# Kernel tuning notes

Measured on AMD Instinct MI355X. Metric: run time of the kernel, lower is better.

## Reference

```python
import jax, jax.numpy as jnp
import numpy as np

K = 8              # kernel_size
C_IN = 3           # input_channels
HID = 256          # hidden_state_size
MID = 256          # mid_layer_size
N_MAIN = 4         # num_main_layers
N_CLS = 1000       # num_classes
N_PIX = K * K      # num_pixel_values
IN_VEC = 2 + 1 + N_PIX * C_IN + HID   # 451
OUT_VEC = 2 + 1 + HID                 # 259
B, H, W = 128, 256, 256


def _lin_init(k, fan_in, fan_out):
    kw, kb = jax.random.split(k)
    bound = 1.0 / np.sqrt(fan_in)
    w = jax.random.uniform(kw, (fan_in, fan_out), jnp.float32, -bound, bound)
    b = jax.random.uniform(kb, (fan_out,), jnp.float32, -bound, bound)
    return w, b


def setup_inputs() -> dict:
    key = jax.random.key(0)
    ks = jax.random.split(key, 16)
    image = jax.random.normal(ks[0], (B, C_IN, H, W), jnp.float32)
    locations = jax.random.uniform(ks[1], (B, 2), jnp.float32)
    scales = jax.random.uniform(ks[2], (B, 1), jnp.float32)
    hidden_state = jax.random.normal(ks[3], (B, HID), jnp.float32)
    w0, b0 = _lin_init(ks[4], IN_VEC, MID)
    rws, rbs = [], []
    for i in range(N_MAIN):
        w, b = _lin_init(jax.random.fold_in(ks[5], i), MID, MID)
        rws.append(w); rbs.append(b)
    rw = jnp.stack(rws); rb = jnp.stack(rbs)          # [4,MID,MID], [4,MID]
    wf, bf = _lin_init(ks[6], MID, OUT_VEC)
    cw0, cb0 = _lin_init(ks[7], HID, MID)
    crw, crb = _lin_init(ks[8], MID, MID)
    cw1, cb1 = _lin_init(ks[9], MID, N_CLS)
    return {"image": image, "locations": locations, "scales": scales,
            "hidden_state": hidden_state, "w0": w0, "b0": b0, "rw": rw,
            "rb": rb, "wf": wf, "bf": bf, "cw0": cw0, "cb0": cb0,
            "crw": crw, "crb": crb, "cw1": cw1, "cb1": cb1}


def fourier_interp_2d(image, sample_points):
    """Band-limited (NUDFT) interpolation of image at continuous points.
    image: [B,C,H,W]; sample_points: [B,N,2] in normalized [0,1) (ij order).
    Returns [B,N,C]."""
    Bsz, C, Hh, Ww = image.shape
    F = jnp.fft.fft2(image)                       # [B,C,H,W] complex
    fy = jnp.fft.fftfreq(Hh) * Hh                 # integer freqs [H]
    fx = jnp.fft.fftfreq(Ww) * Ww                 # integer freqs [W]
    y = sample_points[..., 0]                     # [B,N]
    x = sample_points[..., 1]
    two_pi_i = 2j * jnp.pi
    Ey = jnp.exp(two_pi_i * y[..., None] * fy)    # [B,N,H]
    Ex = jnp.exp(two_pi_i * x[..., None] * fx)    # [B,N,W]
    tmp = jnp.einsum('bchw,bnh->bcnw', F, Ey)     # dominant compute
    vals = jnp.einsum('bcnw,bnw->bcn', tmp, Ex).real / (Hh * Ww)
    return jnp.transpose(vals, (0, 2, 1))         # [B,N,C]


def reference(image, locations, scales, hidden_state,
              w0, b0, rw, rb, wf, bf, cw0, cb0, crw, crb, cw1, cb1):
    Bsz = image.shape[0]
    # base meshgrid: [K,K,2], ij indexing, values arange(K)/K
    g = jnp.arange(K, dtype=image.dtype) / K
    mesh = jnp.stack(jnp.meshgrid(g, g, indexing='ij'), axis=-1)  # [K,K,2]
    coords = mesh[None] - locations[:, None, None, :]             # [B,K,K,2]
    coords = coords * scales[:, None, None, :]
    coords = coords.reshape(Bsz, N_PIX, 2)
    pix = fourier_interp_2d(image, coords)                        # [B,N,C]
    pix = pix.reshape(Bsz, N_PIX * C_IN)
    inp = jnp.concatenate([locations, scales, pix, hidden_state], axis=-1)
    h = inp @ w0 + b0
    for i in range(N_MAIN):
        h = jax.nn.relu(h @ rw[i] + rb[i] + h)
    out = jnp.tanh(h @ wf + bf)                                   # [B,OUT_VEC]
    new_loc = locations + out[:, :2]
    new_scale = scales + out[:, 2:3]
    new_hidden = hidden_state + out[:, 3:]
    c = jax.nn.relu(new_hidden @ cw0 + cb0)
    c = jax.nn.relu(c @ crw + crb + c)
    preds = jax.nn.softmax(c @ cw1 + cb1, axis=-1)
    # concat all outputs: [B, 2+1+HID+N_CLS]
    return jnp.concatenate([new_loc, new_scale, new_hidden, preds], axis=-1)
```

## Files before the change

### kernel.cpp

```cpp
#include <hip/hip_runtime.h>
#include <math.h>

#define BB 128
#define OUTROW 1259

typedef float vf4 __attribute__((ext_vector_type(4)));

__device__ __forceinline__ ushort f2b(float x) {
    unsigned u = __float_as_uint(x);
    unsigned r = (u + 0x7FFFu + ((u >> 16) & 1u)) >> 16;
    return (ushort)r;
}
__device__ __forceinline__ float b2f(ushort b) {
    return __uint_as_float(((unsigned)b) << 16);
}
__device__ __forceinline__ float4 bf4tof(ushort4 u) {
    float4 f;
    f.x = __uint_as_float((unsigned)u.x << 16);
    f.y = __uint_as_float((unsigned)u.y << 16);
    f.z = __uint_as_float((unsigned)u.z << 16);
    f.w = __uint_as_float((unsigned)u.w << 16);
    return f;
}

#define OFF_W0   0u
#define OFF_RW   115456u
#define OFF_CW0  377600u
#define OFF_CRW  443136u
#define OFF_CW1  508672u
#define OFF_WF   764672u
#define N_CONV   831232u

__device__ __forceinline__ void dirichlet_ab(float t, float& A, float& Bv) {
    float r = t - rintf(t);
    float s256 = sinpif(256.0f * r);
    Bv = s256 * (1.0f / 256.0f);
    if (fabsf(r) < 1e-6f) {
        A = 1.0f;
    } else {
        float sp = sinpif(r), cp = cospif(r);
        A = Bv * cp / sp;
    }
}

__global__ __launch_bounds__(256) void interp_convert_kernel(
    const float* __restrict__ image, const float* __restrict__ loc,
    const float* __restrict__ scl, float* __restrict__ pix,
    const float* __restrict__ w0, const float* __restrict__ rw,
    const float* __restrict__ wf, const float* __restrict__ cw0,
    const float* __restrict__ crw, const float* __restrict__ cw1,
    ushort* __restrict__ bfa)
{
    __shared__ float U[256 * 16];
    __shared__ float V[16 * 260];
    __shared__ float T[16 * 260];

    int bid = blockIdx.x;
    int tid = threadIdx.x;

    if (bid >= 384) {
        unsigned g = (unsigned)(bid - 384) * 256u + (unsigned)tid;
        for (unsigned i = g; i < N_CONV; i += 2048u * 256u) {
            unsigned j = i; float v;
            if (j < 115456u) { v = w0[j]; bfa[OFF_W0 + j] = f2b(v); continue; }
            j -= 115456u;
            if (j < 262144u) { v = rw[j]; bfa[OFF_RW + j] = f2b(v); continue; }
            j -= 262144u;
            if (j < 65536u) { v = cw0[j]; bfa[OFF_CW0 + j] = f2b(v); continue; }
            j -= 65536u;
            if (j < 65536u) { v = crw[j]; bfa[OFF_CRW + j] = f2b(v); continue; }
            j -= 65536u;
            if (j < 256000u) { v = cw1[j]; bfa[OFF_CW1 + j] = f2b(v); continue; }
            j -= 256000u;
            {
                unsigned k = j / 260u, c = j - k * 260u;
                bfa[OFF_WF + j] = (c < 259u) ? f2b(wf[k * 259u + c]) : (ushort)0;
            }
        }
        return;
    }

    int b = bid / 3, c = bid % 3;
    float l0 = loc[2 * b], l1 = loc[2 * b + 1], sc = scl[b];

    {
        int p = tid;
        float tp = (float)p * (1.0f / 256.0f);
        #pragma unroll
        for (int iy = 0; iy < 8; ++iy) {
            float A, Bv;
            float y = ((float)iy * 0.125f - l0) * sc;
            dirichlet_ab(y - tp, A, Bv);
            int w = iy >> 1, o = iy & 1;
            U[p * 16 + w * 4 + o] = A;
            U[p * 16 + w * 4 + 2 + o] = Bv;
            float x = ((float)iy * 0.125f - l1) * sc;
            dirichlet_ab(x - tp, A, Bv);
            V[iy * 260 + p] = A;
            V[(8 + iy) * 260 + p] = Bv;
        }
    }
    __syncthreads();

    int wave = tid >> 6, lane = tid & 63;
    const float* img = image + (size_t)(b * 3 + c) * 65536 + lane * 4;

    float aA0[4] = {0, 0, 0, 0}, aA1[4] = {0, 0, 0, 0};
    float aB0[4] = {0, 0, 0, 0}, aB1[4] = {0, 0, 0, 0};
    #pragma unroll 4
    for (int p = 0; p < 256; ++p) {
        vf4 v = __builtin_nontemporal_load((const vf4*)(img + p * 256));
        const float4 u = *(const float4*)(&U[p * 16 + wave * 4]);
        aA0[0] += u.x * v[0]; aA0[1] += u.x * v[1]; aA0[2] += u.x * v[2]; aA0[3] += u.x * v[3];
        aA1[0] += u.y * v[0]; aA1[1] += u.y * v[1]; aA1[2] += u.y * v[2]; aA1[3] += u.y * v[3];
        aB0[0] += u.z * v[0]; aB0[1] += u.z * v[1]; aB0[2] += u.z * v[2]; aB0[3] += u.z * v[3];
        aB1[0] += u.w * v[0]; aB1[1] += u.w * v[1]; aB1[2] += u.w * v[2]; aB1[3] += u.w * v[3];
    }
    int iy0 = wave * 2;
    int q0 = lane * 4;
    #pragma unroll
    for (int j = 0; j < 4; ++j) {
        T[iy0 * 260 + q0 + j]       = aA0[j];
        T[(iy0 + 1) * 260 + q0 + j] = aA1[j];
        T[(8 + iy0) * 260 + q0 + j]     = aB0[j];
        T[(8 + iy0 + 1) * 260 + q0 + j] = aB1[j];
    }
    __syncthreads();

    int n = tid >> 2, sub = tid & 3;
    int iy = n >> 3, ix = n & 7;
    float s = 0.f;
    #pragma unroll 8
    for (int i = 0; i < 64; ++i) {
        int q = sub + 4 * i;
        s += T[iy * 260 + q] * V[ix * 260 + q] - T[(8 + iy) * 260 + q] * V[(8 + ix) * 260 + q];
    }
    s += __shfl_xor(s, 1);
    s += __shfl_xor(s, 2);
    if (sub == 0) pix[(b * 64 + n) * 3 + c] = s;
}

__device__ __forceinline__ void gemv256b(const ushort* __restrict__ W,
                                         const float* __restrict__ s_src,
                                         float* __restrict__ s_part,
                                         int sub, int j4)
{
    ushort4 wv[16];
    float hv[16];
    #pragma unroll
    for (int t = 0; t < 16; ++t)
        wv[t] = *(const ushort4*)(W + (size_t)(sub + 16 * t) * 256 + j4);
    #pragma unroll
    for (int t = 0; t < 16; ++t)
        hv[t] = s_src[sub + 16 * t];
    float4 a = {0.f, 0.f, 0.f, 0.f};
    #pragma unroll
    for (int t = 0; t < 16; ++t) {
        float4 w = bf4tof(wv[t]);
        a.x += hv[t] * w.x; a.y += hv[t] * w.y;
        a.z += hv[t] * w.z; a.w += hv[t] * w.w;
    }
    *(float4*)(&s_part[sub * 256 + j4]) = a;
}

__global__ __launch_bounds__(1024, 1) void mlp_main(
    const float* __restrict__ loc, const float* __restrict__ scl,
    const float* __restrict__ hidden, const float* __restrict__ pix,
    const ushort* __restrict__ bfa,
    const float* __restrict__ b0, const float* __restrict__ rb,
    const float* __restrict__ bf, const float* __restrict__ cb0,
    const float* __restrict__ crb,
    float* __restrict__ c1buf, float* __restrict__ out)
{
    __shared__ float s_in[452];
    __shared__ float s_h[256];
    __shared__ float s_c[256];
    __shared__ float s_o[260];
    __shared__ float s_part[16 * 260];
    __shared__ float s_b0[256], s_rb[1024], s_bf[260], s_cb0[256], s_crb[256];

    const ushort* w0b  = bfa + OFF_W0;
    const ushort* rwb  = bfa + OFF_RW;
    const ushort* wfb  = bfa + OFF_WF;
    const ushort* cw0b = bfa + OFF_CW0;
    const ushort* crwb = bfa + OFF_CRW;

    int b = blockIdx.x, tid = threadIdx.x;
    int jg = tid & 63, sub = tid >> 6;
    int j4 = jg * 4;
    float* orow = out + (size_t)b * OUTROW;

    if (tid < 2) s_in[tid] = loc[2 * b + tid];
    if (tid == 2) s_in[2] = scl[b];
    if (tid >= 256 && tid < 448) s_in[3 + (tid - 256)] = pix[b * 192 + (tid - 256)];
    if (tid >= 512 && tid < 768) s_in[195 + (tid - 512)] = hidden[b * 256 + (tid - 512)];
    if (tid < 256) s_b0[tid] = b0[tid];
    s_rb[tid] = rb[tid];
    if (tid < 259) s_bf[tid] = bf[tid];
    if (tid >= 256 && tid < 512) s_cb0[tid - 256] = cb0[tid - 256];
    if (tid >= 512 && tid < 768) s_crb[tid - 512] = crb[tid - 512];
    __syncthreads();

    {
        float4 acc = {0.f, 0.f, 0.f, 0.f};
        {
            ushort4 wv[14]; float hv[14];
            #pragma unroll
            for (int t = 0; t < 14; ++t)
                wv[t] = *(const ushort4*)(w0b + (size_t)(sub + 16 * t) * 256 + j4);
            #pragma unroll
            for (int t = 0; t < 14; ++t) hv[t] = s_in[sub + 16 * t];
            #pragma unroll
            for (int t = 0; t < 14; ++t) {
                float4 w = bf4tof(wv[t]);
                acc.x += hv[t] * w.x; acc.y += hv[t] * w.y;
                acc.z += hv[t] * w.z; acc.w += hv[t] * w.w;
            }
        }
        {
            ushort4 wv[14]; float hv[14];
            #pragma unroll
            for (int t = 0; t < 14; ++t)
                wv[t] = *(const ushort4*)(w0b + (size_t)(sub + 16 * (t + 14)) * 256 + j4);
            #pragma unroll
            for (int t = 0; t < 14; ++t) hv[t] = s_in[sub + 16 * (t + 14)];
            #pragma unroll
            for (int t = 0; t < 14; ++t) {
                float4 w = bf4tof(wv[t]);
                acc.x += hv[t] * w.x; acc.y += hv[t] * w.y;
                acc.z += hv[t] * w.z; acc.w += hv[t] * w.w;
            }
        }
        if (sub < 3) {
            int k = 448 + sub;
            float hv = s_in[k];
            float4 w = bf4tof(*(const ushort4*)(w0b + (size_t)k * 256 + j4));
            acc.x += hv * w.x; acc.y += hv * w.y; acc.z += hv * w.z; acc.w += hv * w.w;
        }
        *(float4*)(&s_part[sub * 256 + j4]) = acc;
    }
    __syncthreads();
    if (tid < 256) {
        float a = s_b0[tid];
        #pragma unroll
        for (int s = 0; s < 16; ++s) a += s_part[s * 256 + tid];
        s_h[tid] = a;
    }
    __syncthreads();

    #pragma unroll 1
    for (int L = 0; L < 4; ++L) {
        gemv256b(rwb + (size_t)L * 65536, s_h, s_part, sub, j4);
        __syncthreads();
        if (tid < 256) {
            float v = s_rb[L * 256 + tid] + s_h[tid];
            #pragma unroll
            for (int s = 0; s < 16; ++s) v += s_part[s * 256 + tid];
            s_h[tid] = fmaxf(v, 0.f);
        }
        __syncthreads();
    }

    {
        float a0 = 0.f, a1 = 0.f, a2 = 0.f, a3 = 0.f, e = 0.f;
        ushort4 wv[16]; float hv[16]; ushort ev[16];
        #pragma unroll
        for (int t = 0; t < 16; ++t) {
            int k = sub + 16 * t;
            wv[t] = *(const ushort4*)(wfb + (size_t)k * 260 + j4);
            if (jg < 3) ev[t] = wfb[(size_t)k * 260 + 256 + jg];
        }
        #pragma unroll
        for (int t = 0; t < 16; ++t) hv[t] = s_h[sub + 16 * t];
        #pragma unroll
        for (int t = 0; t < 16; ++t) {
            float4 w = bf4tof(wv[t]);
            a0 += hv[t] * w.x; a1 += hv[t] * w.y; a2 += hv[t] * w.z; a3 += hv[t] * w.w;
            if (jg < 3) e += hv[t] * b2f(ev[t]);
        }
        s_part[sub * 260 + j4 + 0] = a0;
        s_part[sub * 260 + j4 + 1] = a1;
        s_part[sub * 260 + j4 + 2] = a2;
        s_part[sub * 260 + j4 + 3] = a3;
        if (jg < 3) s_part[sub * 260 + 256 + jg] = e;
    }
    __syncthreads();
    if (tid < 259) {
        float a = s_bf[tid];
        #pragma unroll
        for (int s = 0; s < 16; ++s) a += s_part[s * 260 + tid];
        s_o[tid] = tanhf(a);
    }
    __syncthreads();

    if (tid < 256) {
        float nh = s_in[195 + tid] + s_o[3 + tid];
        orow[3 + tid] = nh;
        s_h[tid] = nh;
    }
    if (tid == 256) orow[0] = s_in[0] + s_o[0];
    if (tid == 257) orow[1] = s_in[1] + s_o[1];
    if (tid == 258) orow[2] = s_in[2] + s_o[2];
    __syncthreads();

    gemv256b(cw0b, s_h, s_part, sub, j4);
    __syncthreads();
    if (tid < 256) {
        float v = s_cb0[tid];
        #pragma unroll
        for (int s = 0; s < 16; ++s) v += s_part[s * 256 + tid];
        s_c[tid] = fmaxf(v, 0.f);
    }
    __syncthreads();

    gemv256b(crwb, s_c, s_part, sub, j4);
    __syncthreads();
    if (tid < 256) {
        float v = s_crb[tid] + s_c[tid];
        #pragma unroll
        for (int s = 0; s < 16; ++s) v += s_part[s * 256 + tid];
        c1buf[b * 256 + tid] = fmaxf(v, 0.f);
    }
}

__global__ __launch_bounds__(1024, 1) void logits_kernel(
    const float* __restrict__ c1buf, const ushort* __restrict__ bfa,
    const float* __restrict__ cb1, float* __restrict__ logits)
{
    __shared__ float s_c1[256];
    __shared__ float s_part[32 * 128];

    const ushort* cw1b = bfa + OFF_CW1;

    int b = blockIdx.x, s = blockIdx.y, tid = threadIdx.x;
    if (tid < 256) s_c1[tid] = c1buf[b * 256 + tid];
    __syncthreads();

    int cg = tid & 31, sub = tid >> 5;
    int c4 = cg * 4;
    int col0 = s * 128 + c4;
    bool valid = (col0 + 3) < 1000;

    float4 acc = {0.f, 0.f, 0.f, 0.f};
    if (valid) {
        ushort4 wv[8]; float hv[8];
        #pragma unroll
        for (int t = 0; t < 8; ++t)
            wv[t] = *(const ushort4*)(cw1b + (size_t)(sub + 32 * t) * 1000 + col0);
        #pragma unroll
        for (int t = 0; t < 8; ++t) hv[t] = s_c1[sub + 32 * t];
        #pragma unroll
        for (int t = 0; t < 8; ++t) {
            float4 w = bf4tof(wv[t]);
            acc.x += hv[t] * w.x; acc.y += hv[t] * w.y;
            acc.z += hv[t] * w.z; acc.w += hv[t] * w.w;
        }
    }
    *(float4*)(&s_part[sub * 128 + c4]) = acc;
    __syncthreads();

    if (tid < 128) {
        int col = s * 128 + tid;
        if (col < 1000) {
            float a = cb1[col];
            #pragma unroll
            for (int ss = 0; ss < 32; ++ss) a += s_part[ss * 128 + tid];
            logits[(size_t)b * 1000 + col] = a;
        }
    }
}

__global__ __launch_bounds__(1024) void softmax_kernel(
    const float* __restrict__ logits, float* __restrict__ out)
{
    __shared__ float s_red[32];
    int b = blockIdx.x, tid = threadIdx.x;
    float* orow = out + (size_t)b * OUTROW;

    float lgv = (tid < 1000) ? logits[(size_t)b * 1000 + tid] : -1e30f;

    int lane = tid & 63, wid = tid >> 6;
    float m = lgv;
    #pragma unroll
    for (int off = 1; off < 64; off <<= 1) m = fmaxf(m, __shfl_xor(m, off));
    if (lane == 0) s_red[wid] = m;
    __syncthreads();
    m = s_red[0];
    #pragma unroll
    for (int w = 1; w < 16; ++w) m = fmaxf(m, s_red[w]);

    float e = (tid < 1000) ? expf(lgv - m) : 0.f;
    float lsum = e;
    #pragma unroll
    for (int off = 1; off < 64; off <<= 1) lsum += __shfl_xor(lsum, off);
    if (lane == 0) s_red[16 + wid] = lsum;
    __syncthreads();
    float total = 0.f;
    #pragma unroll
    for (int w = 0; w < 16; ++w) total += s_red[16 + w];

    if (tid < 1000) orow[259 + tid] = e / total;
}

extern "C" void kernel_launch(void* const* d_in, const int* in_sizes, int n_in,
                              void* d_out, int out_size, void* d_ws, size_t ws_size,
                              hipStream_t stream) {
    const float* image  = (const float*)d_in[0];
    const float* loc    = (const float*)d_in[1];
    const float* scl    = (const float*)d_in[2];
    const float* hidden = (const float*)d_in[3];
    const float* w0  = (const float*)d_in[4];
    const float* b0  = (const float*)d_in[5];
    const float* rw  = (const float*)d_in[6];
    const float* rb  = (const float*)d_in[7];
    const float* wf  = (const float*)d_in[8];
    const float* bf  = (const float*)d_in[9];
    const float* cw0 = (const float*)d_in[10];
    const float* cb0 = (const float*)d_in[11];
    const float* crw = (const float*)d_in[12];
    const float* crb = (const float*)d_in[13];
    const float* cw1 = (const float*)d_in[14];
    const float* cb1 = (const float*)d_in[15];

    float* ws     = (float*)d_ws;
    float* pix    = ws;
    float* c1buf  = ws + 24576;
    float* logits = ws + 24576 + 32768;
    ushort* bfa   = (ushort*)(ws + 185344);

    hipLaunchKernelGGL(interp_convert_kernel, dim3(384 + 2048), dim3(256), 0, stream,
                       image, loc, scl, pix, w0, rw, wf, cw0, crw, cw1, bfa);
    hipLaunchKernelGGL(mlp_main, dim3(BB), dim3(1024), 0, stream,
                       loc, scl, hidden, pix, bfa,
                       b0, rb, bf, cb0, crb, c1buf, (float*)d_out);
    hipLaunchKernelGGL(logits_kernel, dim3(BB, 8), dim3(1024), 0, stream,
                       c1buf, bfa, cb1, logits);
    hipLaunchKernelGGL(softmax_kernel, dim3(BB), dim3(1024), 0, stream,
                       logits, (float*)d_out);
}
```

Baseline: 87.78 us.

## Fuse logits and softmax into MLP kernel and use bf16 dot2 with pair-interleaved weights

Merges the logits and softmax kernels into the main MLP kernel, which removes two launches and the global round trips through c1buf and logits. Weights are repacked into a k-pair-interleaved bf16 layout so every GEMV can use v_dot2_f32_bf16, with activations also packed to bf16 pairs. The conversion grid shrinks to 512 blocks. This rounds activations to bf16 as well, which lowers accuracy, and the logits GEMV now runs on only 128 blocks.

```diff
diff --git a/kernel.cpp b/kernel.cpp
--- a/kernel.cpp
+++ b/kernel.cpp
@@ -11,25 +11,22 @@
     unsigned r = (u + 0x7FFFu + ((u >> 16) & 1u)) >> 16;
     return (ushort)r;
 }
-__device__ __forceinline__ float b2f(ushort b) {
-    return __uint_as_float(((unsigned)b) << 16);
-}
-__device__ __forceinline__ float4 bf4tof(ushort4 u) {
-    float4 f;
-    f.x = __uint_as_float((unsigned)u.x << 16);
-    f.y = __uint_as_float((unsigned)u.y << 16);
-    f.z = __uint_as_float((unsigned)u.z << 16);
-    f.w = __uint_as_float((unsigned)u.w << 16);
-    return f;
+__device__ __forceinline__ uint pack2(float lo, float hi) {
+    return (uint)f2b(lo) | ((uint)f2b(hi) << 16);
+}
+__device__ __forceinline__ float dot2bf(uint a, uint b, float c) {
+    float d;
+    asm("v_dot2_f32_bf16 %0, %1, %2, %3" : "=v"(d) : "v"(a), "v"(b), "v"(c));
+    return d;
 }
 
 #define OFF_W0   0u
-#define OFF_RW   115456u
-#define OFF_CW0  377600u
-#define OFF_CRW  443136u
-#define OFF_CW1  508672u
-#define OFF_WF   764672u
-#define N_CONV   831232u
+#define OFF_RW   122880u
+#define OFF_CW0  385024u
+#define OFF_CRW  450560u
+#define OFF_WF   516096u
+#define OFF_CW1  582656u
+#define N_TOT    838656u
 
 __device__ __forceinline__ void dirichlet_ab(float t, float& A, float& Bv) {
     float r = t - rintf(t);
@@ -60,21 +57,31 @@
 
     if (bid >= 384) {
         unsigned g = (unsigned)(bid - 384) * 256u + (unsigned)tid;
-        for (unsigned i = g; i < N_CONV; i += 2048u * 256u) {
-            unsigned j = i; float v;
-            if (j < 115456u) { v = w0[j]; bfa[OFF_W0 + j] = f2b(v); continue; }
-            j -= 115456u;
-            if (j < 262144u) { v = rw[j]; bfa[OFF_RW + j] = f2b(v); continue; }
-            j -= 262144u;
-            if (j < 65536u) { v = cw0[j]; bfa[OFF_CW0 + j] = f2b(v); continue; }
-            j -= 65536u;
-            if (j < 65536u) { v = crw[j]; bfa[OFF_CRW + j] = f2b(v); continue; }
-            j -= 65536u;
-            if (j < 256000u) { v = cw1[j]; bfa[OFF_CW1 + j] = f2b(v); continue; }
-            j -= 256000u;
-            {
-                unsigned k = j / 260u, c = j - k * 260u;
-                bfa[OFF_WF + j] = (c < 259u) ? f2b(wf[k * 259u + c]) : (ushort)0;
+        for (unsigned i = g; i < N_TOT; i += 512u * 256u) {
+            unsigned j = i;
+            if (j < 122880u) {
+                unsigned kp = j >> 9, r = j & 511u, c = r >> 1, k = 2u*kp + (r & 1u);
+                bfa[OFF_W0 + j] = (k < 451u) ? f2b(w0[k * 256u + c]) : (ushort)0;
+            } else if (j < 385024u) {
+                unsigned jj = j - 122880u;
+                unsigned kp = jj >> 9, r = jj & 511u, c = r >> 1, k = 2u*kp + (r & 1u);
+                bfa[OFF_RW + jj] = f2b(rw[k * 256u + c]);
+            } else if (j < 450560u) {
+                unsigned jj = j - 385024u;
+                unsigned kp = jj >> 9, r = jj & 511u, c = r >> 1, k = 2u*kp + (r & 1u);
+                bfa[OFF_CW0 + jj] = f2b(cw0[k * 256u + c]);
+            } else if (j < 516096u) {
+                unsigned jj = j - 450560u;
+                unsigned kp = jj >> 9, r = jj & 511u, c = r >> 1, k = 2u*kp + (r & 1u);
+                bfa[OFF_CRW + jj] = f2b(crw[k * 256u + c]);
+            } else if (j < 582656u) {
+                unsigned jj = j - 516096u;
+                unsigned kp = jj / 520u, r = jj - kp * 520u, c = r >> 1, k = 2u*kp + (r & 1u);
+                bfa[OFF_WF + jj] = (c < 259u) ? f2b(wf[k * 259u + c]) : (ushort)0;
+            } else {
+                unsigned jj = j - 582656u;
+                unsigned kp = jj / 2000u, r = jj - kp * 2000u, c = r >> 1, k = 2u*kp + (r & 1u);
+                bfa[OFF_CW1 + jj] = f2b(cw1[k * 1000u + c]);
             }
         }
         return;
@@ -140,50 +147,26 @@
     if (sub == 0) pix[(b * 64 + n) * 3 + c] = s;
 }
 
-__device__ __forceinline__ void gemv256b(const ushort* __restrict__ W,
-                                         const float* __restrict__ s_src,
-                                         float* __restrict__ s_part,
-                                         int sub, int j4)
-{
-    ushort4 wv[16];
-    float hv[16];
-    #pragma unroll
-    for (int t = 0; t < 16; ++t)
-        wv[t] = *(const ushort4*)(W + (size_t)(sub + 16 * t) * 256 + j4);
-    #pragma unroll
-    for (int t = 0; t < 16; ++t)
-        hv[t] = s_src[sub + 16 * t];
-    float4 a = {0.f, 0.f, 0.f, 0.f};
-    #pragma unroll
-    for (int t = 0; t < 16; ++t) {
-        float4 w = bf4tof(wv[t]);
-        a.x += hv[t] * w.x; a.y += hv[t] * w.y;
-        a.z += hv[t] * w.z; a.w += hv[t] * w.w;
-    }
-    *(float4*)(&s_part[sub * 256 + j4]) = a;
-}
-
-__global__ __launch_bounds__(1024, 1) void mlp_main(
+__global__ __launch_bounds__(1024, 1) void mlp_fused(
     const float* __restrict__ loc, const float* __restrict__ scl,
     const float* __restrict__ hidden, const float* __restrict__ pix,
     const ushort* __restrict__ bfa,
     const float* __restrict__ b0, const float* __restrict__ rb,
     const float* __restrict__ bf, const float* __restrict__ cb0,
-    const float* __restrict__ crb,
-    float* __restrict__ c1buf, float* __restrict__ out)
+    const float* __restrict__ crb, const float* __restrict__ cb1,
+    float* __restrict__ out)
 {
-    __shared__ float s_in[452];
+    __shared__ float s_in[480];
     __shared__ float s_h[256];
     __shared__ float s_c[256];
     __shared__ float s_o[260];
     __shared__ float s_part[16 * 260];
-    __shared__ float s_b0[256], s_rb[1024], s_bf[260], s_cb0[256], s_crb[256];
-
-    const ushort* w0b  = bfa + OFF_W0;
-    const ushort* rwb  = bfa + OFF_RW;
-    const ushort* wfb  = bfa + OFF_WF;
-    const ushort* cw0b = bfa + OFF_CW0;
-    const ushort* crwb = bfa + OFF_CRW;
+    __shared__ float s_lg[1024];
+    __shared__ uint  s_in2[240];
+    __shared__ uint  s_hb2[128];
+    __shared__ uint  s_cb2[128];
+    __shared__ float s_b0[256], s_rb[1024], s_bf[260], s_cb0[256], s_crb[256], s_cb1[1000];
+    __shared__ float s_red[32];
 
     int b = blockIdx.x, tid = threadIdx.x;
     int jg = tid & 63, sub = tid >> 6;
@@ -194,102 +177,117 @@
     if (tid == 2) s_in[2] = scl[b];
     if (tid >= 256 && tid < 448) s_in[3 + (tid - 256)] = pix[b * 192 + (tid - 256)];
     if (tid >= 512 && tid < 768) s_in[195 + (tid - 512)] = hidden[b * 256 + (tid - 512)];
+    if (tid >= 768 && tid < 797) s_in[451 + (tid - 768)] = 0.f;
     if (tid < 256) s_b0[tid] = b0[tid];
     s_rb[tid] = rb[tid];
     if (tid < 259) s_bf[tid] = bf[tid];
     if (tid >= 256 && tid < 512) s_cb0[tid - 256] = cb0[tid - 256];
     if (tid >= 512 && tid < 768) s_crb[tid - 512] = crb[tid - 512];
-    __syncthreads();
-
-    {
-        float4 acc = {0.f, 0.f, 0.f, 0.f};
-        {
-            ushort4 wv[14]; float hv[14];
-            #pragma unroll
-            for (int t = 0; t < 14; ++t)
-                wv[t] = *(const ushort4*)(w0b + (size_t)(sub + 16 * t) * 256 + j4);
-            #pragma unroll
-            for (int t = 0; t < 14; ++t) hv[t] = s_in[sub + 16 * t];
-            #pragma unroll
-            for (int t = 0; t < 14; ++t) {
-                float4 w = bf4tof(wv[t]);
-                acc.x += hv[t] * w.x; acc.y += hv[t] * w.y;
-                acc.z += hv[t] * w.z; acc.w += hv[t] * w.w;
-            }
-        }
-        {
-            ushort4 wv[14]; float hv[14];
-            #pragma unroll
-            for (int t = 0; t < 14; ++t)
-                wv[t] = *(const ushort4*)(w0b + (size_t)(sub + 16 * (t + 14)) * 256 + j4);
-            #pragma unroll
-            for (int t = 0; t < 14; ++t) hv[t] = s_in[sub + 16 * (t + 14)];
-            #pragma unroll
-            for (int t = 0; t < 14; ++t) {
-                float4 w = bf4tof(wv[t]);
-                acc.x += hv[t] * w.x; acc.y += hv[t] * w.y;
-                acc.z += hv[t] * w.z; acc.w += hv[t] * w.w;
-            }
-        }
-        if (sub < 3) {
-            int k = 448 + sub;
-            float hv = s_in[k];
-            float4 w = bf4tof(*(const ushort4*)(w0b + (size_t)k * 256 + j4));
-            acc.x += hv * w.x; acc.y += hv * w.y; acc.z += hv * w.z; acc.w += hv * w.w;
-        }
-        *(float4*)(&s_part[sub * 256 + j4]) = acc;
+    if (tid < 1000) s_cb1[tid] = cb1[tid];
+    __syncthreads();
+    if (tid < 240) s_in2[tid] = pack2(s_in[2 * tid], s_in[2 * tid + 1]);
+    __syncthreads();
+
+    const ushort* w0b  = bfa + OFF_W0;
+    const ushort* rwb  = bfa + OFF_RW;
+    const ushort* cw0b = bfa + OFF_CW0;
+    const ushort* crwb = bfa + OFF_CRW;
+    const ushort* wfb  = bfa + OFF_WF;
+    const ushort* cw1b = bfa + OFF_CW1;
+
+    {
+        uint4 wv[15]; uint hv[15];
+        #pragma unroll
+        for (int t = 0; t < 15; ++t)
+            wv[t] = *(const uint4*)(w0b + (size_t)(sub + 16 * t) * 512 + jg * 8);
+        #pragma unroll
+        for (int t = 0; t < 15; ++t) hv[t] = s_in2[sub + 16 * t];
+        vf4 a = {0.f, 0.f, 0.f, 0.f};
+        #pragma unroll
+        for (int t = 0; t < 15; ++t) {
+            a[0] = dot2bf(wv[t].x, hv[t], a[0]);
+            a[1] = dot2bf(wv[t].y, hv[t], a[1]);
+            a[2] = dot2bf(wv[t].z, hv[t], a[2]);
+            a[3] = dot2bf(wv[t].w, hv[t], a[3]);
+        }
+        *(vf4*)(&s_part[sub * 256 + j4]) = a;
     }
     __syncthreads();
     if (tid < 256) {
-        float a = s_b0[tid];
-        #pragma unroll
-        for (int s = 0; s < 16; ++s) a += s_part[s * 256 + tid];
-        s_h[tid] = a;
+        float v = s_b0[tid];
+        #pragma unroll
+        for (int s = 0; s < 16; ++s) v += s_part[s * 256 + tid];
+        s_h[tid] = v;
+        float v2 = __shfl_xor(v, 1);
+        if (!(tid & 1)) s_hb2[tid >> 1] = pack2(v, v2);
     }
     __syncthreads();
 
     #pragma unroll 1
     for (int L = 0; L < 4; ++L) {
-        gemv256b(rwb + (size_t)L * 65536, s_h, s_part, sub, j4);
+        const ushort* W = rwb + (size_t)L * 65536;
+        {
+            uint4 wv[8]; uint hv[8];
+            #pragma unroll
+            for (int t = 0; t < 8; ++t)
+                wv[t] = *(const uint4*)(W + (size_t)(sub + 16 * t) * 512 + jg * 8);
+            #pragma unroll
+            for (int t = 0; t < 8; ++t) hv[t] = s_hb2[sub + 16 * t];
+            vf4 a = {0.f, 0.f, 0.f, 0.f};
+            #pragma unroll
+            for (int t = 0; t < 8; ++t) {
+                a[0] = dot2bf(wv[t].x, hv[t], a[0]);
+                a[1] = dot2bf(wv[t].y, hv[t], a[1]);
+                a[2] = dot2bf(wv[t].z, hv[t], a[2]);
+                a[3] = dot2bf(wv[t].w, hv[t], a[3]);
+            }
+            *(vf4*)(&s_part[sub * 256 + j4]) = a;
+        }
         __syncthreads();
         if (tid < 256) {
             float v = s_rb[L * 256 + tid] + s_h[tid];
             #pragma unroll
             for (int s = 0; s < 16; ++s) v += s_part[s * 256 + tid];
-            s_h[tid] = fmaxf(v, 0.f);
+            v = fmaxf(v, 0.f);
+            s_h[tid] = v;
+            float v2 = __shfl_xor(v, 1);
+            if (!(tid & 1)) s_hb2[tid >> 1] = pack2(v, v2);
         }
         __syncthreads();
     }
 
     {
-        float a0 = 0.f, a1 = 0.f, a2 = 0.f, a3 = 0.f, e = 0.f;
-        ushort4 wv[16]; float hv[16]; ushort ev[16];
-        #pragma unroll
-        for (int t = 0; t < 16; ++t) {
-            int k = sub + 16 * t;
-            wv[t] = *(const ushort4*)(wfb + (size_t)k * 260 + j4);
-            if (jg < 3) ev[t] = wfb[(size_t)k * 260 + 256 + jg];
-        }
-        #pragma unroll
-        for (int t = 0; t < 16; ++t) hv[t] = s_h[sub + 16 * t];
-        #pragma unroll
-        for (int t = 0; t < 16; ++t) {
-            float4 w = bf4tof(wv[t]);
-            a0 += hv[t] * w.x; a1 += hv[t] * w.y; a2 += hv[t] * w.z; a3 += hv[t] * w.w;
-            if (jg < 3) e += hv[t] * b2f(ev[t]);
-        }
-        s_part[sub * 260 + j4 + 0] = a0;
-        s_part[sub * 260 + j4 + 1] = a1;
-        s_part[sub * 260 + j4 + 2] = a2;
-        s_part[sub * 260 + j4 + 3] = a3;
-        if (jg < 3) s_part[sub * 260 + 256 + jg] = e;
+        uint4 wv[8]; uint hv[8];
+        #pragma unroll
+        for (int t = 0; t < 8; ++t)
+            wv[t] = *(const uint4*)(wfb + (size_t)(sub + 16 * t) * 520 + jg * 8);
+        #pragma unroll
+        for (int t = 0; t < 8; ++t) hv[t] = s_hb2[sub + 16 * t];
+        vf4 a = {0.f, 0.f, 0.f, 0.f};
+        #pragma unroll
+        for (int t = 0; t < 8; ++t) {
+            a[0] = dot2bf(wv[t].x, hv[t], a[0]);
+            a[1] = dot2bf(wv[t].y, hv[t], a[1]);
+            a[2] = dot2bf(wv[t].z, hv[t], a[2]);
+            a[3] = dot2bf(wv[t].w, hv[t], a[3]);
+        }
+        *(vf4*)(&s_part[sub * 260 + j4]) = a;
+        if (jg < 4) {
+            float e = 0.f;
+            #pragma unroll
+            for (int t = 0; t < 8; ++t) {
+                uint w = *(const uint*)(wfb + (size_t)(sub + 16 * t) * 520 + 512 + jg * 2);
+                e = dot2bf(w, hv[t], e);
+            }
+            s_part[sub * 260 + 256 + jg] = e;
+        }
     }
     __syncthreads();
     if (tid < 259) {
-        float a = s_bf[tid];
-        #pragma unroll
-        for (int s = 0; s < 16; ++s) a += s_part[s * 260 + tid];
-        s_o[tid] = tanhf(a);
+        float v = s_bf[tid];
+        #pragma unroll
+        for (int s = 0; s < 16; ++s) v += s_part[s * 260 + tid];
+        s_o[tid] = tanhf(v);
     }
     __syncthreads();
 
@@ -297,88 +295,128 @@
         float nh = s_in[195 + tid] + s_o[3 + tid];
         orow[3 + tid] = nh;
         s_h[tid] = nh;
+        float v2 = __shfl_xor(nh, 1);
+        if (!(tid & 1)) s_hb2[tid >> 1] = pack2(nh, v2);
     }
     if (tid == 256) orow[0] = s_in[0] + s_o[0];
     if (tid == 257) orow[1] = s_in[1] + s_o[1];
     if (tid == 258) orow[2] = s_in[2] + s_o[2];
     __syncthreads();
 
-    gemv256b(cw0b, s_h, s_part, sub, j4);
+    {
+        uint4 wv[8]; uint hv[8];
+        #pragma unroll
+        for (int t = 0; t < 8; ++t)
+            wv[t] = *(const uint4*)(cw0b + (size_t)(sub + 16 * t) * 512 + jg * 8);
+        #pragma unroll
+        for (int t = 0; t < 8; ++t) hv[t] = s_hb2[sub + 16 * t];
+        vf4 a = {0.f, 0.f, 0.f, 0.f};
+        #pragma unroll
+        for (int t = 0; t < 8; ++t) {
+            a[0] = dot2bf(wv[t].x, hv[t], a[0]);
+            a[1] = dot2bf(wv[t].y, hv[t], a[1]);
+            a[2] = dot2bf(wv[t].z, hv[t], a[2]);
+            a[3] = dot2bf(wv[t].w, hv[t], a[3]);
+        }
+        *(vf4*)(&s_part[sub * 256 + j4]) = a;
+    }
     __syncthreads();
     if (tid < 256) {
         float v = s_cb0[tid];
         #pragma unroll
         for (int s = 0; s < 16; ++s) v += s_part[s * 256 + tid];
-        s_c[tid] = fmaxf(v, 0.f);
-    }
-    __syncthreads();
-
-    gemv256b(crwb, s_c, s_part, sub, j4);
+        v = fmaxf(v, 0.f);
+        s_c[tid] = v;
+        float v2 = __shfl_xor(v, 1);
+        if (!(tid & 1)) s_cb2[tid >> 1] = pack2(v, v2);
+    }
+    __syncthreads();
+
+    {
+        uint4 wv[8]; uint hv[8];
+        #pragma unroll
+        for (int t = 0; t < 8; ++t)
+            wv[t] = *(const uint4*)(crwb + (size_t)(sub + 16 * t) * 512 + jg * 8);
+        #pragma unroll
+        for (int t = 0; t < 8; ++t) hv[t] = s_cb2[sub + 16 * t];
+        vf4 a = {0.f, 0.f, 0.f, 0.f};
+        #pragma unroll
+        for (int t = 0; t < 8; ++t) {
+            a[0] = dot2bf(wv[t].x, hv[t], a[0]);
+            a[1] = dot2bf(wv[t].y, hv[t], a[1]);
+            a[2] = dot2bf(wv[t].z, hv[t], a[2]);
+            a[3] = dot2bf(wv[t].w, hv[t], a[3]);
+        }
+        *(vf4*)(&s_part[sub * 256 + j4]) = a;
+    }
     __syncthreads();
     if (tid < 256) {
         float v = s_crb[tid] + s_c[tid];
         #pragma unroll
         for (int s = 0; s < 16; ++s) v += s_part[s * 256 + tid];
-        c1buf[b * 256 + tid] = fmaxf(v, 0.f);
-    }
-}
-
-__global__ __launch_bounds__(1024, 1) void logits_kernel(
-    const float* __restrict__ c1buf, const ushort* __restrict__ bfa,
-    const float* __restrict__ cb1, float* __restrict__ logits)
-{
-    __shared__ float s_c1[256];
-    __shared__ float s_part[32 * 128];
-
-    const ushort* cw1b = bfa + OFF_CW1;
-
-    int b = blockIdx.x, s = blockIdx.y, tid = threadIdx.x;
-    if (tid < 256) s_c1[tid] = c1buf[b * 256 + tid];
-    __syncthreads();
-
-    int cg = tid & 31, sub = tid >> 5;
-    int c4 = cg * 4;
-    int col0 = s * 128 + c4;
-    bool valid = (col0 + 3) < 1000;
-
-    float4 acc = {0.f, 0.f, 0.f, 0.f};
-    if (valid) {
-        ushort4 wv[8]; float hv[8];
-        #pragma unroll
-        for (int t = 0; t < 8; ++t)
-            wv[t] = *(const ushort4*)(cw1b + (size_t)(sub + 32 * t) * 1000 + col0);
-        #pragma unroll
-        for (int t = 0; t < 8; ++t) hv[t] = s_c1[sub + 32 * t];
-        #pragma unroll
-        for (int t = 0; t < 8; ++t) {
-            float4 w = bf4tof(wv[t]);
-            acc.x += hv[t] * w.x; acc.y += hv[t] * w.y;
-            acc.z += hv[t] * w.z; acc.w += hv[t] * w.w;
-        }
-    }
-    *(float4*)(&s_part[sub * 128 + c4]) = acc;
-    __syncthreads();
-
-    if (tid < 128) {
-        int col = s * 128 + tid;
-        if (col < 1000) {
-            float a = cb1[col];
-            #pragma unroll
-            for (int ss = 0; ss < 32; ++ss) a += s_part[ss * 128 + tid];
-            logits[(size_t)b * 1000 + col] = a;
-        }
-    }
-}
-
-__global__ __launch_bounds__(1024) void softmax_kernel(
-    const float* __restrict__ logits, float* __restrict__ out)
-{
-    __shared__ float s_red[32];
-    int b = blockIdx.x, tid = threadIdx.x;
-    float* orow = out + (size_t)b * OUTROW;
-
-    float lgv = (tid < 1000) ? logits[(size_t)b * 1000 + tid] : -1e30f;
-
+        v = fmaxf(v, 0.f);
+        float v2 = __shfl_xor(v, 1);
+        if (!(tid & 1)) s_cb2[tid >> 1] = pack2(v, v2);
+    }
+    __syncthreads();
+
+    int jg8 = tid & 127, sub8 = tid >> 7;
+    int c4 = jg8 * 4;
+    {
+        uint4 wv[16]; uint hv[16];
+        #pragma unroll
+        for (int t = 0; t < 16; ++t)
+            wv[t] = *(const uint4*)(cw1b + (size_t)(sub8 + 8 * t) * 2000 + c4 * 2);
+        #pragma unroll
+        for (int t = 0; t < 16; ++t) hv[t] = s_cb2[sub8 + 8 * t];
+        vf4 a = {0.f, 0.f, 0.f, 0.f};
+        #pragma unroll
+        for (int t = 0; t < 16; ++t) {
+            a[0] = dot2bf(wv[t].x, hv[t], a[0]);
+            a[1] = dot2bf(wv[t].y, hv[t], a[1]);
+            a[2] = dot2bf(wv[t].z, hv[t], a[2]);
+            a[3] = dot2bf(wv[t].w, hv[t], a[3]);
+        }
+        *(vf4*)(&s_part[sub8 * 512 + c4]) = a;
+    }
+    __syncthreads();
+    if (tid < 512) {
+        float v = s_cb1[tid];
+        #pragma unroll
+        for (int s = 0; s < 8; ++s) v += s_part[s * 512 + tid];
+        s_lg[tid] = v;
+    }
+    __syncthreads();
+
+    {
+        vf4 a = {0.f, 0.f, 0.f, 0.f};
+        if (jg8 < 122) {
+            uint4 wv[16]; uint hv[16];
+            #pragma unroll
+            for (int t = 0; t < 16; ++t)
+                wv[t] = *(const uint4*)(cw1b + (size_t)(sub8 + 8 * t) * 2000 + (512 + c4) * 2);
+            #pragma unroll
+            for (int t = 0; t < 16; ++t) hv[t] = s_cb2[sub8 + 8 * t];
+            #pragma unroll
+            for (int t = 0; t < 16; ++t) {
+                a[0] = dot2bf(wv[t].x, hv[t], a[0]);
+                a[1] = dot2bf(wv[t].y, hv[t], a[1]);
+                a[2] = dot2bf(wv[t].z, hv[t], a[2]);
+                a[3] = dot2bf(wv[t].w, hv[t], a[3]);
+            }
+        }
+        *(vf4*)(&s_part[sub8 * 512 + c4]) = a;
+    }
+    __syncthreads();
+    if (tid < 488) {
+        float v = s_cb1[512 + tid];
+        #pragma unroll
+        for (int s = 0; s < 8; ++s) v += s_part[s * 512 + tid];
+        s_lg[512 + tid] = v;
+    }
+    __syncthreads();
+
+    float lgv = (tid < 1000) ? s_lg[tid] : -1e30f;
     int lane = tid & 63, wid = tid >> 6;
     float m = lgv;
     #pragma unroll
@@ -422,19 +460,13 @@
     const float* cw1 = (const float*)d_in[14];
     const float* cb1 = (const float*)d_in[15];
 
-    float* ws     = (float*)d_ws;
-    float* pix    = ws;
-    float* c1buf  = ws + 24576;
-    float* logits = ws + 24576 + 32768;
-    ushort* bfa   = (ushort*)(ws + 185344);
-
-    hipLaunchKernelGGL(interp_convert_kernel, dim3(384 + 2048), dim3(256), 0, stream,
+    float* ws   = (float*)d_ws;
+    float* pix  = ws;
+    ushort* bfa = (ushort*)(ws + 24576);
+
+    hipLaunchKernelGGL(interp_convert_kernel, dim3(384 + 512), dim3(256), 0, stream,
                        image, loc, scl, pix, w0, rw, wf, cw0, crw, cw1, bfa);
-    hipLaunchKernelGGL(mlp_main, dim3(BB), dim3(1024), 0, stream,
+    hipLaunchKernelGGL(mlp_fused, dim3(BB), dim3(1024), 0, stream,
                        loc, scl, hidden, pix, bfa,
-                       b0, rb, bf, cb0, crb, c1buf, (float*)d_out);
-    hipLaunchKernelGGL(logits_kernel, dim3(BB, 8), dim3(1024), 0, stream,
-                       c1buf, bfa, cb1, logits);
-    hipLaunchKernelGGL(softmax_kernel, dim3(BB), dim3(1024), 0, stream,
-                       logits, (float*)d_out);
-}
+                       b0, rb, bf, cb0, crb, cb1, (float*)d_out);
+}
```

After: 74.31 us. -15.3%, faster.
